# Kernel optimization log

Measured on AMD Instinct MI355X. Metric: run time of the kernel, lower is better.

## Reference

```python
import jax, jax.numpy as jnp
import numpy as np

B, C, H, W = 16, 128, 128, 128
CO = C // 2  # conv output channels


def _binary_activation(x):
    # forward: sign(x); backward: piecewise-polynomial surrogate (STE)
    out_fwd = jnp.sign(x)
    m1 = (x < -1).astype(x.dtype)
    m2 = (x < 0).astype(x.dtype)
    m3 = (x < 1).astype(x.dtype)
    out1 = -1.0 * m1 + (x * x + 2.0 * x) * (1.0 - m1)
    out2 = out1 * m2 + (-x * x + 2.0 * x) * (1.0 - m2)
    out3 = out2 * m3 + 1.0 * (1.0 - m3)
    return jax.lax.stop_gradient(out_fwd) - jax.lax.stop_gradient(out3) + out3


def _binary_weights(conv_w):
    w = conv_w.reshape(CO, C, 3, 3)
    # per-output-channel mean(|w|), detached
    sf = jax.lax.stop_gradient(jnp.mean(jnp.abs(w), axis=(1, 2, 3), keepdims=True))
    bw_ng = sf * jnp.sign(w)
    wc = jnp.clip(w, -1.0, 1.0)
    return jax.lax.stop_gradient(bw_ng) - jax.lax.stop_gradient(wc) + wc


def setup_inputs() -> dict:
    key = jax.random.key(0)
    k1, k2, k3 = jax.random.split(key, 3)
    x = jax.random.normal(k1, (B, C, H, W), dtype=jnp.float32)
    bias1 = jnp.zeros((1, C, 1, 1), dtype=jnp.float32)
    prelu_a = jnp.full((1, C, 1, 1), 0.25, dtype=jnp.float32)
    bias2 = jnp.zeros((1, C, 1, 1), dtype=jnp.float32)
    # stored flat like HardBinaryConv.weights; zero-mean so signs are mixed
    conv_w = jax.random.normal(k2, (CO * C * 9, 1), dtype=jnp.float32) * 0.001
    # grouped 1x1 conv: groups=CO, 2 input channels per group
    pool_w = jax.random.normal(k3, (CO, 2, 1, 1), dtype=jnp.float32) * 0.1
    return {"x": x, "bias1": bias1, "prelu_a": prelu_a, "bias2": bias2,
            "conv_w": conv_w, "pool_w": pool_w}


def reference(x, bias1, prelu_a, bias2, conv_w, pool_w):
    b, c, h, w = x.shape
    co = c // 2
    out = x + bias1
    out = jnp.maximum(out, 0.0) + prelu_a * jnp.minimum(out, 0.0)  # PReLU per-channel
    out = out + bias2
    out = _binary_activation(out)
    bw = _binary_weights(conv_w)
    y = jax.lax.conv_general_dilated(out, bw, window_strides=(1, 1),
                                     padding=((1, 1), (1, 1)),
                                     dimension_numbers=("NCHW", "OIHW", "NCHW"))
    # grouped 1x1 channel pool: out chan o = w[o,0]*x[2o] + w[o,1]*x[2o+1]
    shortcut = jnp.sum(x.reshape(b, co, 2, h, w) * pool_w.reshape(1, co, 2, 1, 1), axis=2)
    y = y + shortcut
    # PixelUnshuffle(2): (B,co,H,W) -> (B,4*co,H/2,W/2)
    ho, wo = h // 2, w // 2
    y = y.reshape(b, co, ho, 2, wo, 2).transpose(0, 1, 3, 5, 2, 4).reshape(b, co * 4, ho, wo)
    return y
```

## Files before the change

### kernel.cpp

```cpp
#include <hip/hip_runtime.h>
#include <stdint.h>

typedef __attribute__((ext_vector_type(4))) float f32x4;
typedef __attribute__((ext_vector_type(4))) unsigned int u32x4;
typedef __attribute__((ext_vector_type(4))) int i32x4;

#define NB 16
#define NC 128
#define NH 128
#define NW 128
#define WP 130

__device__ __forceinline__ int swz7(int wp) { return (wp ^ (wp >> 3)) & 7; }

__global__ __launch_bounds__(256) void k_prep(const float* __restrict__ cw,
                                              const float* __restrict__ b1,
                                              const float* __restrict__ pa,
                                              const float* __restrict__ b2,
                                              float* __restrict__ sf,
                                              float* __restrict__ theta,
                                              unsigned char* __restrict__ wf) {
    int b = blockIdx.x, t = threadIdx.x;
    int f = b * 256 + t;
    int bb  = f & 15;
    int l   = (f >> 4) & 63;
    int ni  = (f >> 10) & 3;
    int m   = (f >> 12) & 1;
    int p   = f >> 13;
    int o = ni * 16 + (l & 15);
    int c = m * 64 + (l >> 4) * 16 + bb;
    float wv = cw[o * 1152 + c * 9 + p];
    wf[f] = wv > 0.f ? (unsigned char)0x01
                     : (wv < 0.f ? (unsigned char)0xFF : (unsigned char)0x00);
    if (b < 64) {
        __shared__ float red[4];
        const float* pp = cw + b * 1152;
        float s = 0.f;
        for (int i = t; i < 1152; i += 256) s += fabsf(pp[i]);
#pragma unroll
        for (int off = 32; off > 0; off >>= 1) s += __shfl_down(s, off);
        if ((t & 63) == 0) red[t >> 6] = s;
        __syncthreads();
        if (t == 0) sf[b] = (red[0] + red[1] + red[2] + red[3]) * (1.0f / 1152.0f);
    }
    if (b == 64 && t < NC) {
        float B1 = b1[t], A = pa[t], B2 = b2[t];
        theta[t] = (-B2 >= 0.f) ? (-B1 - B2) : (-B1 - B2 / A);
    }
}

__device__ __forceinline__ unsigned int pki8(float v, float th) {
    return v > th ? 0x01u : (v < th ? 0xFFu : 0u);
}

__global__ __launch_bounds__(256, 2) void k_fused(
    const float* __restrict__ x, const float* __restrict__ theta,
    const float* __restrict__ pw, const unsigned char* __restrict__ wf,
    const float* __restrict__ sf, float* __restrict__ out) {
    __shared__ __align__(16) unsigned char AT[69632];
    int bxr = blockIdx.x;
    int bx = (bxr & 7) * 128 + (bxr >> 3);
    int nb = bx >> 6;
    int h2b = bx & 63;
    int t = threadIdx.x;
    int wid = t >> 6;
    int l = t & 63;
    int lr = l & 15, lg = l >> 4;

    if (t < 64) {
        int rho = t >> 4, side = (t >> 3) & 1, u = t & 7;
        int wp = side ? (WP - 1) : 0;
        u32x4 z = {0u, 0u, 0u, 0u};
        *(u32x4*)(AT + (size_t)(rho * WP + wp) * NC + ((u ^ swz7(wp)) << 4)) = z;
    }

    int w4 = t & 31, cg = t >> 5;
    const float* xbase = x + ((size_t)nb * NC + cg * 16) * (NH * NW) + 4 * w4;
    f32x4 th0 = *(const f32x4*)(theta + cg * 16);
    f32x4 th1 = *(const f32x4*)(theta + cg * 16 + 4);
    f32x4 th2 = *(const f32x4*)(theta + cg * 16 + 8);
    f32x4 th3 = *(const f32x4*)(theta + cg * 16 + 12);
    f32x4 p0 = *(const f32x4*)(pw + cg * 16);
    f32x4 p1 = *(const f32x4*)(pw + cg * 16 + 4);
    f32x4 p2 = *(const f32x4*)(pw + cg * 16 + 8);
    f32x4 p3 = *(const f32x4*)(pw + cg * 16 + 12);
    float pwv[16] = {p0.x, p0.y, p0.z, p0.w, p1.x, p1.y, p1.z, p1.w,
                     p2.x, p2.y, p2.z, p2.w, p3.x, p3.y, p3.z, p3.w};
    float sc0[8][4], sc1[8][4];
    f32x4 XA[16], XB[16], XC[16];

#define ISSUE(XR, HH) \
    { const float* xp = xbase + (size_t)(HH) * NW; \
      _Pragma("unroll") for (int cc = 0; cc < 16; ++cc) \
          XR[cc] = *(const f32x4*)(xp + (size_t)cc * (NH * NW)); }
#define PACKROWM(RHO, XR, EM) \
    _Pragma("unroll") for (int ww = 0; ww < 4; ++ww) { \
        int wp = 4 * w4 + ww + 1; \
        u32x4 v; \
        v.x = (pki8(XR[0][ww], th0.x) | (pki8(XR[1][ww], th0.y) << 8) | \
               (pki8(XR[2][ww], th0.z) << 16) | (pki8(XR[3][ww], th0.w) << 24)) & (EM); \
        v.y = (pki8(XR[4][ww], th1.x) | (pki8(XR[5][ww], th1.y) << 8) | \
               (pki8(XR[6][ww], th1.z) << 16) | (pki8(XR[7][ww], th1.w) << 24)) & (EM); \
        v.z = (pki8(XR[8][ww], th2.x) | (pki8(XR[9][ww], th2.y) << 8) | \
               (pki8(XR[10][ww], th2.z) << 16) | (pki8(XR[11][ww], th2.w) << 24)) & (EM); \
        v.w = (pki8(XR[12][ww], th3.x) | (pki8(XR[13][ww], th3.y) << 8) | \
               (pki8(XR[14][ww], th3.z) << 16) | (pki8(XR[15][ww], th3.w) << 24)) & (EM); \
        *(u32x4*)(AT + (size_t)((RHO) * WP + wp) * NC + ((cg ^ swz7(wp)) << 4)) = v; \
    }
#define SCROW(SC, XR) \
    _Pragma("unroll") for (int i = 0; i < 8; ++i) { \
        float wa = pwv[2 * i], wb = pwv[2 * i + 1]; \
        _Pragma("unroll") for (int ww = 0; ww < 4; ++ww) \
            SC[i][ww] = wa * XR[2 * i][ww] + wb * XR[2 * i + 1][ww]; \
    }

    int hTop = (h2b > 0) ? (2 * h2b - 1) : 0;
    int hBot = (h2b < 63) ? (2 * h2b + 2) : 127;
    unsigned emT = (h2b > 0) ? 0xFFFFFFFFu : 0u;
    unsigned emB = (h2b < 63) ? 0xFFFFFFFFu : 0u;

    ISSUE(XA, hTop)
    ISSUE(XB, 2 * h2b)
    ISSUE(XC, 2 * h2b + 1)
    __builtin_amdgcn_sched_barrier(0);
    PACKROWM(0, XA, emT)
    ISSUE(XA, hBot)
    __builtin_amdgcn_sched_barrier(0);
    PACKROWM(1, XB, 0xFFFFFFFFu)
    SCROW(sc0, XB)
    PACKROWM(2, XC, 0xFFFFFFFFu)
    SCROW(sc1, XC)
    PACKROWM(3, XA, emB)

    float sfr[4];
#pragma unroll
    for (int ni = 0; ni < 4; ++ni) sfr[ni] = sf[ni * 16 + lr];

    int w0 = (wid & 1) * 64;
    i32x4 acc[4][4];
    i32x4 zero = {0, 0, 0, 0};
#pragma unroll
    for (int mi = 0; mi < 4; ++mi)
#pragma unroll
        for (int ni = 0; ni < 4; ++ni) acc[mi][ni] = zero;
    __syncthreads();

    __builtin_amdgcn_s_setprio(1);
#pragma unroll
    for (int p = 0; p < 9; ++p) {
        int kh = p / 3, kw = p % 3;
        int rho = (wid >> 1) + kh;
        int wp = w0 + kw + lr;
        const unsigned char* ap = AT + (size_t)(rho * WP + wp) * NC;
        const unsigned char* brow = wf + p * 8192 + l * 16;
        i32x4 bfr[2][4];
#pragma unroll
        for (int m = 0; m < 2; ++m)
#pragma unroll
            for (int ni = 0; ni < 4; ++ni)
                bfr[m][ni] = *(const i32x4*)(brow + m * 4096 + ni * 1024);
#pragma unroll
        for (int mi = 0; mi < 4; ++mi) {
            int s7m = swz7(wp + mi * 16);
            i32x4 a0 = *(const i32x4*)(ap + mi * 2048 + ((lg ^ s7m) << 4));
            i32x4 a1 = *(const i32x4*)(ap + mi * 2048 + (((lg + 4) ^ s7m) << 4));
#pragma unroll
            for (int ni = 0; ni < 4; ++ni) {
                acc[mi][ni] = __builtin_amdgcn_mfma_i32_16x16x64_i8(
                    a0, bfr[0][ni], acc[mi][ni], 0, 0, 0);
                acc[mi][ni] = __builtin_amdgcn_mfma_i32_16x16x64_i8(
                    a1, bfr[1][ni], acc[mi][ni], 0, 0, 0);
            }
        }
    }
    __builtin_amdgcn_s_setprio(0);
    __syncthreads();

    float (*Tt)[68] = (float (*)[68])(AT + wid * 17408);
#pragma unroll
    for (int mi = 0; mi < 4; ++mi)
#pragma unroll
        for (int ni = 0; ni < 4; ++ni) {
            f32x4 cv;
            cv.x = (float)acc[mi][ni].x * sfr[ni];
            cv.y = (float)acc[mi][ni].y * sfr[ni];
            cv.z = (float)acc[mi][ni].z * sfr[ni];
            cv.w = (float)acc[mi][ni].w * sfr[ni];
            *(f32x4*)&Tt[ni * 16 + lr][mi * 16 + lg * 4] = cv;
        }
    __syncthreads();

    int wha = w4 >> 4, w4l = w4 & 15;
#define EPIROW(R2, SC) { \
    const float (*Ts)[68] = (const float (*)[68])(AT + ((R2) * 2 + wha) * 17408); \
    float* obr = out + (((size_t)nb * 256 + (R2) * 2) * 64 + h2b) * 64 + 2 * w4; \
    _Pragma("unroll") for (int i = 0; i < 8; ++i) { \
        int o = 8 * cg + i; \
        f32x4 cv = *(const f32x4*)&Ts[o][4 * w4l]; \
        float2 A = {cv.x + SC[i][0], cv.z + SC[i][2]}; \
        float2 B = {cv.y + SC[i][1], cv.w + SC[i][3]}; \
        *(float2*)(obr + (size_t)o * 16384)        = A; \
        *(float2*)(obr + (size_t)o * 16384 + 4096) = B; \
    } }
    EPIROW(0, sc0)
    EPIROW(1, sc1)
}

extern "C" void kernel_launch(void* const* d_in, const int* in_sizes, int n_in,
                              void* d_out, int out_size, void* d_ws, size_t ws_size,
                              hipStream_t stream) {
    const float* x  = (const float*)d_in[0];
    const float* b1 = (const float*)d_in[1];
    const float* pa = (const float*)d_in[2];
    const float* b2 = (const float*)d_in[3];
    const float* cw = (const float*)d_in[4];
    const float* pw = (const float*)d_in[5];
    float* out = (float*)d_out;
    float* sf = (float*)d_ws;
    float* theta = (float*)((char*)d_ws + 256);
    unsigned char* wfr = (unsigned char*)d_ws + 768;

    k_prep<<<288, 256, 0, stream>>>(cw, b1, pa, b2, sf, theta, wfr);
    k_fused<<<1024, 256, 0, stream>>>(x, theta, pw, wfr, sf, out);
}
```

Measured before the change: 75.59 us.

## Interleave row packing with per-kernel-row MFMA groups using lightweight barriers

Splits the 9-tap MFMA loop into three kernel-row groups. Packing of rows 2 and 3 of the binarized activation tile is deferred so it runs between groups, after the rows each group needs are already in shared memory. Full __syncthreads is replaced by a barrier that waits only on LDS counters, so global loads can stay in flight. The aim is to overlap VALU packing with matrix-core work, at the cost of two extra workgroup barriers.

New measurement: 142.6 us. 88.7% more time.

```diff
diff --git a/kernel.cpp b/kernel.cpp
--- a/kernel.cpp
+++ b/kernel.cpp
@@ -12,6 +12,10 @@
 #define WP 130
 
 __device__ __forceinline__ int swz7(int wp) { return (wp ^ (wp >> 3)) & 7; }
+
+#define LBAR() do { asm volatile("s_waitcnt lgkmcnt(0)" ::: "memory"); \
+                    __builtin_amdgcn_s_barrier(); \
+                    __builtin_amdgcn_sched_barrier(0); } while (0)
 
 __global__ __launch_bounds__(256) void k_prep(const float* __restrict__ cw,
                                               const float* __restrict__ b1,
@@ -113,6 +117,29 @@
         _Pragma("unroll") for (int ww = 0; ww < 4; ++ww) \
             SC[i][ww] = wa * XR[2 * i][ww] + wb * XR[2 * i + 1][ww]; \
     }
+#define MFMAG(KH) \
+    _Pragma("unroll") for (int kw = 0; kw < 3; ++kw) { \
+        int p = (KH) * 3 + kw; \
+        int rho = (wid >> 1) + (KH); \
+        int wp = w0 + kw + lr; \
+        const unsigned char* ap = AT + (size_t)(rho * WP + wp) * NC; \
+        const unsigned char* brow = wf + p * 8192 + l * 16; \
+        i32x4 bfr[2][4]; \
+        _Pragma("unroll") for (int m = 0; m < 2; ++m) \
+            _Pragma("unroll") for (int ni = 0; ni < 4; ++ni) \
+                bfr[m][ni] = *(const i32x4*)(brow + m * 4096 + ni * 1024); \
+        _Pragma("unroll") for (int mi = 0; mi < 4; ++mi) { \
+            int s7m = swz7(wp + mi * 16); \
+            i32x4 a0 = *(const i32x4*)(ap + mi * 2048 + ((lg ^ s7m) << 4)); \
+            i32x4 a1 = *(const i32x4*)(ap + mi * 2048 + (((lg + 4) ^ s7m) << 4)); \
+            _Pragma("unroll") for (int ni = 0; ni < 4; ++ni) { \
+                acc[mi][ni] = __builtin_amdgcn_mfma_i32_16x16x64_i8( \
+                    a0, bfr[0][ni], acc[mi][ni], 0, 0, 0); \
+                acc[mi][ni] = __builtin_amdgcn_mfma_i32_16x16x64_i8( \
+                    a1, bfr[1][ni], acc[mi][ni], 0, 0, 0); \
+            } \
+        } \
+    }
 
     int hTop = (h2b > 0) ? (2 * h2b - 1) : 0;
     int hBot = (h2b < 63) ? (2 * h2b + 2) : 127;
@@ -128,9 +155,6 @@
     __builtin_amdgcn_sched_barrier(0);
     PACKROWM(1, XB, 0xFFFFFFFFu)
     SCROW(sc0, XB)
-    PACKROWM(2, XC, 0xFFFFFFFFu)
-    SCROW(sc1, XC)
-    PACKROWM(3, XA, emB)
 
     float sfr[4];
 #pragma unroll
@@ -143,38 +167,23 @@
     for (int mi = 0; mi < 4; ++mi)
 #pragma unroll
         for (int ni = 0; ni < 4; ++ni) acc[mi][ni] = zero;
-    __syncthreads();
-
+
+    LBAR();
     __builtin_amdgcn_s_setprio(1);
-#pragma unroll
-    for (int p = 0; p < 9; ++p) {
-        int kh = p / 3, kw = p % 3;
-        int rho = (wid >> 1) + kh;
-        int wp = w0 + kw + lr;
-        const unsigned char* ap = AT + (size_t)(rho * WP + wp) * NC;
-        const unsigned char* brow = wf + p * 8192 + l * 16;
-        i32x4 bfr[2][4];
-#pragma unroll
-        for (int m = 0; m < 2; ++m)
-#pragma unroll
-            for (int ni = 0; ni < 4; ++ni)
-                bfr[m][ni] = *(const i32x4*)(brow + m * 4096 + ni * 1024);
-#pragma unroll
-        for (int mi = 0; mi < 4; ++mi) {
-            int s7m = swz7(wp + mi * 16);
-            i32x4 a0 = *(const i32x4*)(ap + mi * 2048 + ((lg ^ s7m) << 4));
-            i32x4 a1 = *(const i32x4*)(ap + mi * 2048 + (((lg + 4) ^ s7m) << 4));
-#pragma unroll
-            for (int ni = 0; ni < 4; ++ni) {
-                acc[mi][ni] = __builtin_amdgcn_mfma_i32_16x16x64_i8(
-                    a0, bfr[0][ni], acc[mi][ni], 0, 0, 0);
-                acc[mi][ni] = __builtin_amdgcn_mfma_i32_16x16x64_i8(
-                    a1, bfr[1][ni], acc[mi][ni], 0, 0, 0);
-            }
-        }
-    }
+    MFMAG(0)
     __builtin_amdgcn_s_setprio(0);
-    __syncthreads();
+    PACKROWM(2, XC, 0xFFFFFFFFu)
+    SCROW(sc1, XC)
+    LBAR();
+    __builtin_amdgcn_s_setprio(1);
+    MFMAG(1)
+    __builtin_amdgcn_s_setprio(0);
+    PACKROWM(3, XA, emB)
+    LBAR();
+    __builtin_amdgcn_s_setprio(1);
+    MFMAG(2)
+    __builtin_amdgcn_s_setprio(0);
+    LBAR();
 
     float (*Tt)[68] = (float (*)[68])(AT + wid * 17408);
 #pragma unroll
@@ -188,7 +197,7 @@
             cv.w = (float)acc[mi][ni].w * sfr[ni];
             *(f32x4*)&Tt[ni * 16 + lr][mi * 16 + lg * 4] = cv;
         }
-    __syncthreads();
+    LBAR();
 
     int wha = w4 >> 4, w4l = w4 & 15;
 #define EPIROW(R2, SC) { \
```
